# Kernel tuning notes

Hardware: AMD Instinct MI355X
Metric: run time of the kernel (lower is better)

## Reference

```python
import jax, jax.numpy as jnp
import numpy as np
from jax import lax

T = 256        # sentence length
V = 50000      # vocab
NT = 50        # POS tags
NL = 40        # dependency labels
WD, TD = 300, 100
IN = WD + TD   # 400, LSTM input & hidden size
H = IN
BI = 2 * H     # 800, biLSTM output per token
MI = 2 * BI    # 1600, MLP input/hidden size


def setup_inputs() -> dict:
    key = jax.random.key(0)
    ks = jax.random.split(key, 32)
    s = 0.05
    d = {
        'words': jax.random.randint(ks[0], (T,), 0, V),
        'tags': jax.random.randint(ks[1], (T,), 0, NT),
        'arcs': jax.random.randint(ks[2], (T + 1,), 0, T + 1),
        'h0': jax.random.normal(ks[3], (4, 1, H), jnp.float32),
        'c0': jax.random.normal(ks[4], (4, 1, H), jnp.float32),
        'word_emb': jax.random.normal(ks[5], (V, WD), jnp.float32) * s,
        'tag_emb': jax.random.normal(ks[6], (NT, TD), jnp.float32) * s,
        # LSTM layer 0: input IN; layer 1: input BI. Leading dim 2 = directions (fwd, rev).
        'Wih0': jax.random.normal(ks[7], (2, 4 * H, IN), jnp.float32) * s,
        'Whh0': jax.random.normal(ks[8], (2, 4 * H, H), jnp.float32) * s,
        'bih0': jax.random.normal(ks[9], (2, 4 * H), jnp.float32) * s,
        'bhh0': jax.random.normal(ks[10], (2, 4 * H), jnp.float32) * s,
        'Wih1': jax.random.normal(ks[11], (2, 4 * H, BI), jnp.float32) * s,
        'Whh1': jax.random.normal(ks[12], (2, 4 * H, H), jnp.float32) * s,
        'bih1': jax.random.normal(ks[13], (2, 4 * H), jnp.float32) * s,
        'bhh1': jax.random.normal(ks[14], (2, 4 * H), jnp.float32) * s,
        # arc-score MLP: 1600 -> 1600 -> 1 (Linear, Tanh, Linear)
        'Wa1': jax.random.normal(ks[15], (MI, MI), jnp.float32) * s,
        'ba1': jax.random.normal(ks[16], (MI,), jnp.float32) * s,
        'Wa2': jax.random.normal(ks[17], (1, MI), jnp.float32) * s,
        'ba2': jax.random.normal(ks[18], (1,), jnp.float32) * s,
        # label MLP: 1600 -> 1600 -> 40
        'Wl1': jax.random.normal(ks[19], (MI, MI), jnp.float32) * s,
        'bl1': jax.random.normal(ks[20], (MI,), jnp.float32) * s,
        'Wl2': jax.random.normal(ks[21], (NL, MI), jnp.float32) * s,
        'bl2': jax.random.normal(ks[22], (NL,), jnp.float32) * s,
    }
    return d


def _lstm_dir(x, Wih, Whh, bih, bhh, h, c):
    # x: [T, in]; returns [T, H]. Torch gate order i, f, g, o.
    xg = x @ Wih.T + (bih + bhh)  # precompute input projection: [T, 4H]

    def step(carry, xt):
        h, c = carry
        g = xt + h @ Whh.T
        i, f, gg, o = jnp.split(g, 4, axis=-1)
        i, f, o = jax.nn.sigmoid(i), jax.nn.sigmoid(f), jax.nn.sigmoid(o)
        c = f * c + i * jnp.tanh(gg)
        h = o * jnp.tanh(c)
        return (h, c), h

    (_, _), ys = lax.scan(step, (h, c), xg)
    return ys


def _bilstm_layer(x, Wih, Whh, bih, bhh, h0f, c0f, h0b, c0b):
    fwd = _lstm_dir(x, Wih[0], Whh[0], bih[0], bhh[0], h0f, c0f)
    bwd = _lstm_dir(x[::-1], Wih[1], Whh[1], bih[1], bhh[1], h0b, c0b)[::-1]
    return jnp.concatenate([fwd, bwd], axis=-1)


def _mlp(z, W1, b1, W2, b2):
    return jnp.tanh(z @ W1.T + b1) @ W2.T + b2


def reference(words, tags, arcs, h0, c0, word_emb, tag_emb,
              Wih0, Whh0, bih0, bhh0, Wih1, Whh1, bih1, bhh1,
              Wa1, ba1, Wa2, ba2, Wl1, bl1, Wl2, bl2):
    n = words.shape[0]
    x = jnp.concatenate([word_emb[words], tag_emb[tags]], axis=-1)  # [T, 400]
    x1 = _bilstm_layer(x, Wih0, Whh0, bih0, bhh0, h0[0, 0], c0[0, 0], h0[1, 0], c0[1, 0])
    hV = _bilstm_layer(x1, Wih1, Whh1, bih1, bhh1, h0[2, 0], c0[2, 0], h0[3, 0], c0[3, 0])  # [T, 800]

    # All-pairs arc scores: feats[h, d] = concat(hV[h], hV[d]) -> MLP -> scalar.
    hh = jnp.broadcast_to(hV[:, None, :], (n, n, BI))
    dd = jnp.broadcast_to(hV[None, :, :], (n, n, BI))
    feats = jnp.concatenate([hh, dd], axis=-1)  # [T, T, 1600]
    raw = _mlp(feats, Wa1, ba1, Wa2, ba2)[..., 0]  # [T, T]
    raw = raw * (1.0 - jnp.eye(n, dtype=raw.dtype))  # head == dep left at 0
    scores = jnp.zeros((n + 1, n + 1), raw.dtype).at[1:, 1:].set(raw).at[0, 0].set(1.0)

    # Labels: for token i with gold head h (1-based), concat(hV[i], hV[h-1]); head==0 -> zeros.
    heads = arcs[1:]
    idx = jnp.clip(heads - 1, 0, n - 1)
    lf = jnp.concatenate([hV, hV[idx]], axis=-1)  # [T, 1600]
    lab = _mlp(lf, Wl1, bl1, Wl2, bl2)  # [T, 40]
    lab = jnp.where((heads == 0)[:, None], jnp.zeros_like(lab), lab)
    return (scores, lab)
```

## Files before the change

kernel.cpp:

```cpp
#include <hip/hip_runtime.h>

typedef unsigned int   u32;
typedef unsigned long long u64;

__device__ __forceinline__ float fast_tanh(float x) {
    x = fminf(fmaxf(x, -15.f), 15.f);
    float e = __expf(2.f * x);
    return __fdividef(e - 1.f, e + 1.f);
}

#define HLD(p) __hip_atomic_load((p), __ATOMIC_RELAXED, __HIP_MEMORY_SCOPE_AGENT)

#define OF_XG   ((size_t)0)
#define OF_H    (OF_XG + 3276800)
#define OF_PQ   (OF_H  + 1638400)
#define OF_U    (OF_PQ + 3276800)

struct H4 { u64 v0, v1, v2, v3; const u64* p; u32 want; };

__device__ __forceinline__ H4 h4_issue(const u64* __restrict__ hist, int t, int k, u32 base) {
    H4 h;
    if (k < 400) { h.p = hist + (size_t)t * 400 + k;                          h.want = base + (u32)t + 1u; }
    else         { h.p = hist + 102400 + (size_t)(255 - t) * 400 + (k - 400); h.want = base + (u32)(255 - t) + 1u; }
    h.v0 = HLD(h.p + 0); h.v1 = HLD(h.p + 1); h.v2 = HLD(h.p + 2); h.v3 = HLD(h.p + 3);
    return h;
}

__device__ __forceinline__ float4 h4_fin(H4 h) {
    while ((u32)(h.v0 >> 32) != h.want || (u32)(h.v1 >> 32) != h.want ||
           (u32)(h.v2 >> 32) != h.want || (u32)(h.v3 >> 32) != h.want) {
        __builtin_amdgcn_s_sleep(4);
        h.v0 = HLD(h.p + 0); h.v1 = HLD(h.p + 1); h.v2 = HLD(h.p + 2); h.v3 = HLD(h.p + 3);
    }
    return make_float4(__uint_as_float((u32)h.v0), __uint_as_float((u32)h.v1),
                       __uint_as_float((u32)h.v2), __uint_as_float((u32)h.v3));
}

__device__ __forceinline__ void gate_wait(const u64* __restrict__ w0, const u64* __restrict__ w1,
                                          u32 want0, u32 want1) {
    if (threadIdx.x == 0) {
        for (;;) {
            u32 g0 = (u32)(HLD(w0) >> 32);
            u32 g1 = (u32)(HLD(w1) >> 32);
            if (g0 == want0 && g1 == want1) break;
            __builtin_amdgcn_s_sleep(16);
        }
    }
    __syncthreads();
}

__device__ __forceinline__ void gate_cnt(const u32* __restrict__ c, u32 target) {
    if (threadIdx.x == 0) {
        while (__hip_atomic_load(c, __ATOMIC_RELAXED, __HIP_MEMORY_SCOPE_AGENT) < target)
            __builtin_amdgcn_s_sleep(16);
        (void)__hip_atomic_load(c, __ATOMIC_ACQUIRE, __HIP_MEMORY_SCOPE_AGENT);
    }
    __syncthreads();
}

__device__ __forceinline__ void stage_nb(float (*As)[68], float (*Bs)[68],
                                         int lk, int lr, float4 av, float4 bv) {
    As[lk + 0][lr] = av.x; As[lk + 1][lr] = av.y; As[lk + 2][lr] = av.z; As[lk + 3][lr] = av.w;
    Bs[lk + 0][lr] = bv.x; Bs[lk + 1][lr] = bv.y; Bs[lk + 2][lr] = bv.z; Bs[lk + 3][lr] = bv.w;
}

__device__ __forceinline__ void fma16(float acc[4][4], const float (*As)[68], const float (*Bs)[68],
                                      int tx, int ty) {
    #pragma unroll
    for (int kk = 0; kk < 16; ++kk) {
        float4 a4 = *(const float4*)&As[kk][ty * 4];
        float4 b4 = *(const float4*)&Bs[kk][tx * 4];
        acc[0][0] += a4.x * b4.x; acc[0][1] += a4.x * b4.y; acc[0][2] += a4.x * b4.z; acc[0][3] += a4.x * b4.w;
        acc[1][0] += a4.y * b4.x; acc[1][1] += a4.y * b4.y; acc[1][2] += a4.y * b4.z; acc[1][3] += a4.y * b4.w;
        acc[2][0] += a4.z * b4.x; acc[2][1] += a4.z * b4.y; acc[2][2] += a4.z * b4.z; acc[2][3] += a4.z * b4.w;
        acc[3][0] += a4.w * b4.x; acc[3][1] += a4.w * b4.y; acc[3][2] += a4.w * b4.z; acc[3][3] += a4.w * b4.w;
    }
}

__device__ __forceinline__ void gemm_seg(float (*AsB)[16][68], float (*BsB)[16][68],
        float acc[4][4], const u64* __restrict__ hist, int t, int tind, u32 base,
        const float* __restrict__ brow, int kb, int klen,
        int lk, int lr, int tx, int ty, int& pb)
{
    int ka = kb + lk;
    H4 h = h4_issue(hist, ka < 800 ? t : tind, ka < 800 ? ka : ka - 800, base);
    float4 bv = *(const float4*)(brow + ka);
    for (int k0 = kb; k0 < kb + klen; k0 += 16) {
        float4 av = h4_fin(h);
        stage_nb(AsB[pb], BsB[pb], lk, lr, av, bv);
        int kn = k0 + 16;
        if (kn < kb + klen) {
            int k2 = kn + lk;
            h  = h4_issue(hist, k2 < 800 ? t : tind, k2 < 800 ? k2 : k2 - 800, base);
            bv = *(const float4*)(brow + k2);
        }
        __syncthreads();
        fma16(acc, AsB[pb], BsB[pb], tx, ty);
        pb ^= 1;
    }
}

__global__ __launch_bounds__(256)
void gemm_embed_kernel(const int* __restrict__ words, const int* __restrict__ tags,
                       const float* __restrict__ wemb, const float* __restrict__ temb,
                       const float* __restrict__ B,
                       const float* __restrict__ bias1, const float* __restrict__ bias2,
                       float* __restrict__ C, u32* __restrict__ cnt) {
    int t0 = blockIdx.x * 64;
    int n0 = blockIdx.y * 64;
    int tid = threadIdx.x;
    if (blockIdx.x == 0 && blockIdx.y == 0 && tid < 4) cnt[tid] = 0u;
    int tx = tid & 15, ty = tid >> 4;
    int lr = tid >> 2, lk = (tid & 3) * 4;
    __shared__ float As[2][16][68];
    __shared__ float Bs[2][16][68];
    float acc[4][4] = {};

    int t = t0 + lr;
    const float* arow0 = wemb + (size_t)words[t] * 300;
    const float* arow1 = temb + (size_t)tags[t] * 100 - 300;
    const float* brow  = B + (size_t)(n0 + lr) * 400;

    int p = 0;
    float4 av, bv;
    { int k = lk; av = (k < 300) ? *(const float4*)(arow0 + k) : *(const float4*)(arow1 + k);
      bv = *(const float4*)(brow + k); }
    for (int k0 = 0; k0 < 400; k0 += 16) {
        stage_nb(As[p], Bs[p], lk, lr, av, bv);
        int kn = k0 + 16;
        if (kn < 400) {
            int k = kn + lk;
            av = (k < 300) ? *(const float4*)(arow0 + k) : *(const float4*)(arow1 + k);
            bv = *(const float4*)(brow + k);
        }
        __syncthreads();
        fma16(acc, As[p], Bs[p], tx, ty);
        p ^= 1;
    }
    float bs[4];
    #pragma unroll
    for (int j = 0; j < 4; ++j) {
        int n = n0 + tx * 4 + j;
        bs[j] = bias1[n] + bias2[n];
    }
    #pragma unroll
    for (int i = 0; i < 4; ++i) {
        int tr = t0 + ty * 4 + i;
        float4 o;
        o.x = acc[i][0] + bs[0]; o.y = acc[i][1] + bs[1];
        o.z = acc[i][2] + bs[2]; o.w = acc[i][3] + bs[3];
        *(float4*)(C + (size_t)tr * 3200 + n0 + tx * 4) = o;
    }
}

#define LSTM_G 50
__device__ __forceinline__ void lstm_body(int bid,
                 const float* __restrict__ Whh,
                 const float* __restrict__ h0,
                 const float* __restrict__ c0,
                 int hc_base,
                 const float* __restrict__ xg,
                 u64* __restrict__ hist,
                 u32 tag_base,
                 float (*hbuf)[416],
                 const u32* __restrict__ cnt) {
    const int T = 256;
    int d  = bid / LSTM_G;
    int wg = bid % LSTM_G;
    int a8 = wg * 8;
    int tid = threadIdx.x;
    int w = tid >> 6, lane = tid & 63;
    int c = lane & 7, r = lane >> 3;
    int gate = r >> 1, jj = r & 1;
    int gr = gate * 400 + a8 + 2 * w + jj;

    float4 wv[13];
    const float* wrow = Whh + (size_t)d * 640000 + (size_t)gr * 400;
    #pragma unroll
    for (int i = 0; i < 13; ++i) {
        int k = 4 * (c + 8 * i);
        wv[i] = (k + 3 < 400) ? *(const float4*)(wrow + k) : make_float4(0.f, 0.f, 0.f, 0.f);
    }
    if (tid < 16) { hbuf[0][400 + tid] = 0.f; hbuf[1][400 + tid] = 0.f; }

    float c_state = 0.f;
    if (lane == 0 || lane == 8)
        c_state = c0[(hc_base + d) * 400 + a8 + 2 * w + jj];

    if (cnt) { gate_cnt(&cnt[0], 50); gate_cnt(&cnt[1], 50); gate_cnt(&cnt[2], 50); gate_cnt(&cnt[3], 50); }

    u64* hst = hist + (size_t)d * 102400;
    bool need2 = (tid + 256 < 400);

    for (int t = 0; t < T; ++t) {
        int xt = d ? (T - 1 - t) : t;
        float xgv = xg[(size_t)xt * 3200 + d * 1600 + gr];
        float* hb = hbuf[t & 1];

        if (t == 0) {
            hb[tid] = h0[(hc_base + d) * 400 + tid];
            if (need2) hb[tid + 256] = h0[(hc_base + d) * 400 + tid + 256];
        } else {
            const u64* src = hst + (size_t)(t - 1) * 400;
            u32 want = tag_base + (u32)t;
            bool d1 = false, d2 = !need2;
            while (!(d1 && d2)) {
                u64 v1 = 0, v2 = 0;
                if (!d1) v1 = HLD(&src[tid]);
                if (!d2) v2 = HLD(&src[tid + 256]);
                if (!d1 && (u32)(v1 >> 32) == want) { hb[tid] = __uint_as_float((u32)v1); d1 = true; }
                if (!d2 && (u32)(v2 >> 32) == want) { hb[tid + 256] = __uint_as_float((u32)v2); d2 = true; }
            }
        }
        __syncthreads();

        const float4* h4 = (const float4*)hb;
        float s = 0.f;
        #pragma unroll
        for (int i = 0; i < 13; ++i) {
            float4 hv = h4[c + 8 * i];
            s += wv[i].x * hv.x + wv[i].y * hv.y + wv[i].z * hv.z + wv[i].w * hv.w;
        }
        s += __shfl_down(s, 4);
        s += __shfl_down(s, 2);
        s += __shfl_down(s, 1);

        float v = 0.f;
        if (c == 0) {
            float tot = s + xgv;
            float arg = (gate == 2) ? 2.f * tot : -tot;
            arg = fminf(fmaxf(arg, -60.f), 60.f);
            float e = __expf(arg);
            v = (gate == 2) ? (e - 1.f) * __frcp_rn(e + 1.f)
                            : __frcp_rn(1.f + e);
        }
        float fv = __shfl(v, lane + 16);
        float gv = __shfl(v, lane + 32);
        float ov = __shfl(v, lane + 48);
        if (lane == 0 || lane == 8) {
            c_state = fv * c_state + v * gv;
            float ec = __expf(fminf(fmaxf(2.f * c_state, -60.f), 60.f));
            float th = (ec - 1.f) * __frcp_rn(ec + 1.f);
            float h = ov * th;
            u64 pk = (((u64)(tag_base + t + 1)) << 32) | (u64)__float_as_uint(h);
            __hip_atomic_store(&hst[(size_t)t * 400 + a8 + 2 * w + jj], pk,
                               __ATOMIC_RELAXED, __HIP_MEMORY_SCOPE_AGENT);
        }
    }
}

union SmemU {
    struct { float As[2][16][68]; float Bs[2][16][68]; } g;
    float hbuf[2][416];
};

__global__ __launch_bounds__(256)
void mega_kernel(const float* __restrict__ Whh0, const float* __restrict__ Whh1,
                 const float* __restrict__ h0, const float* __restrict__ c0,
                 const float* __restrict__ xg0, float* __restrict__ xg1,
                 u64* __restrict__ hist, const int* __restrict__ arcs,
                 const float* __restrict__ Wih1, const float* __restrict__ bih1,
                 const float* __restrict__ bhh1,
                 const float* __restrict__ Wa1, const float* __restrict__ ba1,
                 const float* __restrict__ Wl1, const float* __restrict__ bl1,
                 float* __restrict__ PQ, float* __restrict__ U, u32* __restrict__ cnt) {
    __shared__ SmemU sm;
    int bid = blockIdx.x;
    int tid = threadIdx.x;

    if (bid < 100) {
        lstm_body(bid, Whh0, h0, c0, 0, xg0, hist, 0u, sm.hbuf, nullptr);
        return;
    }
    if (bid < 300) {
        int g = bid - 100;
        int t0 = (g & 3) * 64;
        int n0 = (g >> 2) * 64;
        int tx = tid & 15, ty = tid >> 4;
        int lr = tid >> 2, lk = (tid & 3) * 4;
        float acc[4][4] = {};
        int t = t0 + lr;
        const float* brow = Wih1 + (size_t)(n0 + lr) * 800;

        int first = (t0 >= 128) ? 400 : 0;
        int pb = 0;
        for (int seg = 0; seg < 2; ++seg) {
            int kb = first ^ (seg ? 400 : 0);
            if (kb == 0) {
                const u64* gw = hist + (size_t)(t0 + 63) * 400;
                gate_wait(gw, gw + 399, (u32)(t0 + 64), (u32)(t0 + 64));
            } else {
                const u64* gw = hist + 102400 + (size_t)(255 - t0) * 400;
                gate_wait(gw, gw + 399, (u32)(256 - t0), (u32)(256 - t0));
            }
            gemm_seg(sm.g.As, sm.g.Bs, acc, hist, t, t, 0u, brow, kb, 400, lk, lr, tx, ty, pb);
        }
        float bs[4];
        #pragma unroll
        for (int j = 0; j < 4; ++j) {
            int n = n0 + tx * 4 + j;
            bs[j] = bih1[n] + bhh1[n];
        }
        #pragma unroll
        for (int i = 0; i < 4; ++i) {
            int tr = t0 + ty * 4 + i;
            float4 o;
            o.x = acc[i][0] + bs[0]; o.y = acc[i][1] + bs[1];
            o.z = acc[i][2] + bs[2]; o.w = acc[i][3] + bs[3];
            *(float4*)(xg1 + (size_t)tr * 3200 + n0 + tx * 4) = o;
        }
        __syncthreads();
        if (tid == 0)
            __hip_atomic_fetch_add(&cnt[t0 >> 6], 1u, __ATOMIC_RELEASE, __HIP_MEMORY_SCOPE_AGENT);
        return;
    }
    if (bid < 400) {
        lstm_body(bid - 300, Whh1, h0, c0, 2, xg1, hist, 256u, sm.hbuf, cnt);
        return;
    }

    gate_cnt(&cnt[0], 50); gate_cnt(&cnt[1], 50); gate_cnt(&cnt[2], 50); gate_cnt(&cnt[3], 50);

    int tx = tid & 15, ty = tid >> 4;
    int lr = tid >> 2, lk = (tid & 3) * 4;
    float acc[4][4] = {};
    int pb = 0;

    if (bid < 500) {
        int g = bid - 400;
        int t0 = (g & 3) * 64;
        int n0 = (g >> 2) * 64;
        int t = t0 + lr;
        int first = (t0 >= 128) ? 400 : 0;
        int h = arcs[1 + t];
        int tind = min(max(h - 1, 0), 255);
        const float* brow = Wl1 + (size_t)(n0 + lr) * 1600;
        for (int seg = 0; seg < 3; ++seg) {
            int kb   = (seg < 2) ? (first ^ (seg ? 400 : 0)) : 800;
            int klen = (seg < 2) ? 400 : 800;
            if (seg < 2) {
                if (kb == 0) {
                    const u64* gw = hist + (size_t)(t0 + 63) * 400;
                    gate_wait(gw, gw + 399, (u32)(t0 + 320), (u32)(t0 + 320));
                } else {
                    const u64* gw = hist + 102400 + (size_t)(255 - t0) * 400;
                    gate_wait(gw, gw + 399, (u32)(512 - t0), (u32)(512 - t0));
                }
            } else {
                const u64* gf = hist + (size_t)255 * 400;
                const u64* gb = hist + 102400 + (size_t)255 * 400;
                gate_wait(gf, gb, 512u, 512u);
            }
            gemm_seg(sm.g.As, sm.g.Bs, acc, hist, t, tind, 256u, brow, kb, klen, lk, lr, tx, ty, pb);
        }
        float bs[4];
        #pragma unroll
        for (int j = 0; j < 4; ++j) bs[j] = bl1[n0 + tx * 4 + j];
        #pragma unroll
        for (int i = 0; i < 4; ++i) {
            int tr = t0 + ty * 4 + i;
            float4 o;
            o.x = fast_tanh(acc[i][0] + bs[0]); o.y = fast_tanh(acc[i][1] + bs[1]);
            o.z = fast_tanh(acc[i][2] + bs[2]); o.w = fast_tanh(acc[i][3] + bs[3]);
            *(float4*)(U + (size_t)tr * 1600 + n0 + tx * 4) = o;
        }
    } else {
        int g = bid - 500;
        int t0 = (g & 3) * 64;
        int n0 = (g >> 2) * 64;
        int t = t0 + lr;
        int first = (t0 >= 128) ? 400 : 0;
        int nn = n0 + lr;
        const float* brow = (nn < 1600) ? Wa1 + (size_t)nn * 1600
                                        : Wa1 + (size_t)(nn - 1600) * 1600 + 800;
        for (int seg = 0; seg < 2; ++seg) {
            int kb = first ^ (seg ? 400 : 0);
            if (kb == 0) {
                const u64* gw = hist + (size_t)(t0 + 63) * 400;
                gate_wait(gw, gw + 399, (u32)(t0 + 320), (u32)(t0 + 320));
            } else {
                const u64* gw = hist + 102400 + (size_t)(255 - t0) * 400;
                gate_wait(gw, gw + 399, (u32)(512 - t0), (u32)(512 - t0));
            }
            gemm_seg(sm.g.As, sm.g.Bs, acc, hist, t, t, 256u, brow, kb, 400, lk, lr, tx, ty, pb);
        }
        float bs[4];
        #pragma unroll
        for (int j = 0; j < 4; ++j) {
            int n = n0 + tx * 4 + j;
            bs[j] = (n < 1600) ? ba1[n] : 0.f;
        }
        #pragma unroll
        for (int i = 0; i < 4; ++i) {
            int tr = t0 + ty * 4 + i;
            float4 o;
            o.x = acc[i][0] + bs[0]; o.y = acc[i][1] + bs[1];
            o.z = acc[i][2] + bs[2]; o.w = acc[i][3] + bs[3];
            *(float4*)(PQ + (size_t)tr * 3200 + n0 + tx * 4) = o;
        }
    }
}

__global__ __launch_bounds__(256)
void arc_kernel(const float* __restrict__ PQ,
                const float* __restrict__ Wa2, const float* __restrict__ ba2,
                float* __restrict__ out) {
    int i0 = blockIdx.x * 8, j0 = blockIdx.y * 8;
    int tid = threadIdx.x;
    __shared__ float Pt[8][66], Qt[8][66];
    __shared__ float W2f[1600];
    __shared__ float part[4][64];

    if (blockIdx.x == 0 && blockIdx.y == 0) {
        if (tid < 257) out[tid] = (tid == 0) ? 1.0f : 0.0f;
        out[(size_t)(tid + 1) * 257] = 0.0f;
        if (tid == 0) out[0] = 1.0f;
    }
    for (int m = tid; m < 1600; m += 256) W2f[m] = Wa2[m];

    int out_i = tid & 63, ii = out_i >> 3, jj = out_i & 7, mc = tid >> 6;
    int slr = tid >> 5, slc = (tid & 31) * 2;
    float acc = 0.f;
    for (int m0 = 0; m0 < 1600; m0 += 64) {
        float2 pv = *(const float2*)(PQ + (size_t)(i0 + slr) * 3200 + m0 + slc);
        float2 qv = *(const float2*)(PQ + (size_t)(j0 + slr) * 3200 + 1600 + m0 + slc);
        __syncthreads();
        Pt[slr][slc] = pv.x; Pt[slr][slc + 1] = pv.y;
        Qt[slr][slc] = qv.x; Qt[slr][slc + 1] = qv.y;
        __syncthreads();
        #pragma unroll
        for (int mm = 0; mm < 16; ++mm) {
            int m = mc * 16 + mm;
            float s = Pt[ii][m] + Qt[jj][m];
            acc += W2f[m0 + m] * fast_tanh(s);
        }
    }
    part[mc][out_i] = acc;
    __syncthreads();
    if (tid < 64) {
        float raw = part[0][tid] + part[1][tid] + part[2][tid] + part[3][tid] + ba2[0];
        int gi = i0 + (tid >> 3), gj = j0 + (tid & 7);
        if (gi == gj) raw = 0.f;
        out[(size_t)(gi + 1) * 257 + (gj + 1)] = raw;
    }
}

__global__ __launch_bounds__(256)
void label_out_kernel(const float* __restrict__ U, const float* __restrict__ Wl2,
                      const float* __restrict__ bl2, const int* __restrict__ arcs,
                      float* __restrict__ out) {
    int t = blockIdx.x;
    __shared__ float u_l[1600];
    __shared__ float part[4][64];
    for (int m = threadIdx.x; m < 1600; m += 256) u_l[m] = U[(size_t)t * 1600 + m];
    __syncthreads();
    int tid = threadIdx.x;
    int n = tid & 63, p = tid >> 6;
    float acc = 0.f;
    if (n < 40) {
        const float4* wr4 = (const float4*)(Wl2 + (size_t)n * 1600 + p * 400);
        const float*  ub  = u_l + p * 400;
        for (int m = 0; m < 100; ++m) {
            float4 w = wr4[m];
            acc += ub[4*m] * w.x + ub[4*m+1] * w.y + ub[4*m+2] * w.z + ub[4*m+3] * w.w;
        }
    }
    part[p][n] = acc;
    __syncthreads();
    if (tid < 40) {
        float v = part[0][tid] + part[1][tid] + part[2][tid] + part[3][tid] + bl2[tid];
        if (arcs[1 + t] == 0) v = 0.f;
        out[(size_t)t * 40 + tid] = v;
    }
}

extern "C" void kernel_launch(void* const* d_in, const int* in_sizes, int n_in,
                              void* d_out, int out_size, void* d_ws, size_t ws_size,
                              hipStream_t stream) {
    const int*   words = (const int*)d_in[0];
    const int*   tags  = (const int*)d_in[1];
    const int*   arcs  = (const int*)d_in[2];
    const float* h0    = (const float*)d_in[3];
    const float* c0    = (const float*)d_in[4];
    const float* wemb  = (const float*)d_in[5];
    const float* temb  = (const float*)d_in[6];
    const float* Wih0  = (const float*)d_in[7];
    const float* Whh0  = (const float*)d_in[8];
    const float* bih0  = (const float*)d_in[9];
    const float* bhh0  = (const float*)d_in[10];
    const float* Wih1  = (const float*)d_in[11];
    const float* Whh1  = (const float*)d_in[12];
    const float* bih1  = (const float*)d_in[13];
    const float* bhh1  = (const float*)d_in[14];
    const float* Wa1   = (const float*)d_in[15];
    const float* ba1   = (const float*)d_in[16];
    const float* Wa2   = (const float*)d_in[17];
    const float* ba2   = (const float*)d_in[18];
    const float* Wl1   = (const float*)d_in[19];
    const float* bl1   = (const float*)d_in[20];
    const float* Wl2   = (const float*)d_in[21];
    const float* bl2   = (const float*)d_in[22];
    float* out = (float*)d_out;

    char* ws = (char*)d_ws;
    float* xg0  = (float*)(ws + OF_XG);
    u64*   hist = (u64*)  (ws + OF_H);
    float* xg1  = (float*)(ws + OF_PQ);
    float* PQ   = (float*)(ws + OF_XG);
    float* U    = (float*)(ws + OF_U);
    u32*   cnt  = (u32*)out + 66040;

    gemm_embed_kernel<<<dim3(4, 50), 256, 0, stream>>>(words, tags, wemb, temb, Wih0, bih0, bhh0, xg0, cnt);
    mega_kernel<<<700, 256, 0, stream>>>(Whh0, Whh1, h0, c0, xg0, xg1, hist, arcs,
                                         Wih1, bih1, bhh1, Wa1, ba1, Wl1, bl1, PQ, U, cnt);
    arc_kernel<<<dim3(32, 32), 256, 0, stream>>>(PQ, Wa2, ba2, out);
    label_out_kernel<<<256, 256, 0, stream>>>(U, Wl2, bl2, arcs, out + 66049);
}
```

Before: 1.137 ms.

## Fuse layer-0 input GEMM into mega kernel and split label MLP into per-token halves

The embedding and layer-0 input-projection GEMM moves into the persistent mega kernel as 200 extra blocks, each bumping a per-time-tile counter. The layer-0 LSTM waits on those counters per 64-step tile, so the recurrence can begin before the whole GEMM finishes. The label MLP first layer is rewritten the same way as the arc MLP: separate left and right projections per token, gathered and passed through tanh in the label output kernel. This drops the gated 800-wide gather segment and lets the label GEMM blocks run with the same two-segment schedule. The cost is a memset launch, a larger grid that depends on co-residency for the spin-waits, and a doubled label projection output.

New measurement: 1.129 ms. About the same (-0.8%).

```diff
diff --git a/kernel.cpp b/kernel.cpp
--- a/kernel.cpp
+++ b/kernel.cpp
@@ -14,7 +14,6 @@
 #define OF_XG   ((size_t)0)
 #define OF_H    (OF_XG + 3276800)
 #define OF_PQ   (OF_H  + 1638400)
-#define OF_U    (OF_PQ + 3276800)
 
 struct H4 { u64 v0, v1, v2, v3; const u64* p; u32 want; };
 
@@ -100,59 +99,6 @@
     }
 }
 
-__global__ __launch_bounds__(256)
-void gemm_embed_kernel(const int* __restrict__ words, const int* __restrict__ tags,
-                       const float* __restrict__ wemb, const float* __restrict__ temb,
-                       const float* __restrict__ B,
-                       const float* __restrict__ bias1, const float* __restrict__ bias2,
-                       float* __restrict__ C, u32* __restrict__ cnt) {
-    int t0 = blockIdx.x * 64;
-    int n0 = blockIdx.y * 64;
-    int tid = threadIdx.x;
-    if (blockIdx.x == 0 && blockIdx.y == 0 && tid < 4) cnt[tid] = 0u;
-    int tx = tid & 15, ty = tid >> 4;
-    int lr = tid >> 2, lk = (tid & 3) * 4;
-    __shared__ float As[2][16][68];
-    __shared__ float Bs[2][16][68];
-    float acc[4][4] = {};
-
-    int t = t0 + lr;
-    const float* arow0 = wemb + (size_t)words[t] * 300;
-    const float* arow1 = temb + (size_t)tags[t] * 100 - 300;
-    const float* brow  = B + (size_t)(n0 + lr) * 400;
-
-    int p = 0;
-    float4 av, bv;
-    { int k = lk; av = (k < 300) ? *(const float4*)(arow0 + k) : *(const float4*)(arow1 + k);
-      bv = *(const float4*)(brow + k); }
-    for (int k0 = 0; k0 < 400; k0 += 16) {
-        stage_nb(As[p], Bs[p], lk, lr, av, bv);
-        int kn = k0 + 16;
-        if (kn < 400) {
-            int k = kn + lk;
-            av = (k < 300) ? *(const float4*)(arow0 + k) : *(const float4*)(arow1 + k);
-            bv = *(const float4*)(brow + k);
-        }
-        __syncthreads();
-        fma16(acc, As[p], Bs[p], tx, ty);
-        p ^= 1;
-    }
-    float bs[4];
-    #pragma unroll
-    for (int j = 0; j < 4; ++j) {
-        int n = n0 + tx * 4 + j;
-        bs[j] = bias1[n] + bias2[n];
-    }
-    #pragma unroll
-    for (int i = 0; i < 4; ++i) {
-        int tr = t0 + ty * 4 + i;
-        float4 o;
-        o.x = acc[i][0] + bs[0]; o.y = acc[i][1] + bs[1];
-        o.z = acc[i][2] + bs[2]; o.w = acc[i][3] + bs[3];
-        *(float4*)(C + (size_t)tr * 3200 + n0 + tx * 4) = o;
-    }
-}
-
 #define LSTM_G 50
 __device__ __forceinline__ void lstm_body(int bid,
                  const float* __restrict__ Whh,
@@ -163,7 +109,8 @@
                  u64* __restrict__ hist,
                  u32 tag_base,
                  float (*hbuf)[416],
-                 const u32* __restrict__ cnt) {
+                 const u32* __restrict__ cntPre,
+                 const u32* __restrict__ cntXg) {
     const int T = 256;
     int d  = bid / LSTM_G;
     int wg = bid % LSTM_G;
@@ -187,12 +134,17 @@
     if (lane == 0 || lane == 8)
         c_state = c0[(hc_base + d) * 400 + a8 + 2 * w + jj];
 
-    if (cnt) { gate_cnt(&cnt[0], 50); gate_cnt(&cnt[1], 50); gate_cnt(&cnt[2], 50); gate_cnt(&cnt[3], 50); }
+    if (cntPre) { gate_cnt(&cntPre[0], 50); gate_cnt(&cntPre[1], 50);
+                  gate_cnt(&cntPre[2], 50); gate_cnt(&cntPre[3], 50); }
 
     u64* hst = hist + (size_t)d * 102400;
     bool need2 = (tid + 256 < 400);
 
     for (int t = 0; t < T; ++t) {
+        if (cntXg && (t & 63) == 0) {
+            int tile = d ? 3 - (t >> 6) : (t >> 6);
+            gate_cnt(&cntXg[tile], 50);
+        }
         int xt = d ? (T - 1 - t) : t;
         float xgv = xg[(size_t)xt * 3200 + d * 1600 + gr];
         float* hb = hbuf[t & 1];
@@ -255,29 +207,80 @@
 };
 
 __global__ __launch_bounds__(256)
-void mega_kernel(const float* __restrict__ Whh0, const float* __restrict__ Whh1,
+void mega_kernel(const int* __restrict__ words, const int* __restrict__ tags,
+                 const float* __restrict__ wemb, const float* __restrict__ temb,
+                 const float* __restrict__ Wih0, const float* __restrict__ bih0,
+                 const float* __restrict__ bhh0,
+                 const float* __restrict__ Whh0, const float* __restrict__ Whh1,
                  const float* __restrict__ h0, const float* __restrict__ c0,
-                 const float* __restrict__ xg0, float* __restrict__ xg1,
+                 float* __restrict__ xg0, float* __restrict__ xg1,
                  u64* __restrict__ hist, const int* __restrict__ arcs,
                  const float* __restrict__ Wih1, const float* __restrict__ bih1,
                  const float* __restrict__ bhh1,
                  const float* __restrict__ Wa1, const float* __restrict__ ba1,
-                 const float* __restrict__ Wl1, const float* __restrict__ bl1,
-                 float* __restrict__ PQ, float* __restrict__ U, u32* __restrict__ cnt) {
+                 const float* __restrict__ Wl1,
+                 float* __restrict__ PQ, float* __restrict__ ULVR,
+                 u32* __restrict__ cnt) {
     __shared__ SmemU sm;
     int bid = blockIdx.x;
     int tid = threadIdx.x;
-
-    if (bid < 100) {
-        lstm_body(bid, Whh0, h0, c0, 0, xg0, hist, 0u, sm.hbuf, nullptr);
+    int tx = tid & 15, ty = tid >> 4;
+    int lr = tid >> 2, lk = (tid & 3) * 4;
+
+    if (bid < 200) {
+        int ttile, nt;
+        if (bid < 100) { ttile = (bid & 1) * 3;  nt = bid >> 1; }
+        else           { ttile = 1 + (bid & 1);  nt = (bid - 100) >> 1; }
+        int t0 = ttile * 64, n0 = nt * 64;
+        float acc[4][4] = {};
+        int t = t0 + lr;
+        const float* arow0 = wemb + (size_t)words[t] * 300;
+        const float* arow1 = temb + (size_t)tags[t] * 100 - 300;
+        const float* brow  = Wih0 + (size_t)(n0 + lr) * 400;
+
+        int p = 0;
+        float4 av, bv;
+        { int k = lk; av = (k < 300) ? *(const float4*)(arow0 + k) : *(const float4*)(arow1 + k);
+          bv = *(const float4*)(brow + k); }
+        for (int k0 = 0; k0 < 400; k0 += 16) {
+            stage_nb(sm.g.As[p], sm.g.Bs[p], lk, lr, av, bv);
+            int kn = k0 + 16;
+            if (kn < 400) {
+                int k = kn + lk;
+                av = (k < 300) ? *(const float4*)(arow0 + k) : *(const float4*)(arow1 + k);
+                bv = *(const float4*)(brow + k);
+            }
+            __syncthreads();
+            fma16(acc, sm.g.As[p], sm.g.Bs[p], tx, ty);
+            p ^= 1;
+        }
+        float bs[4];
+        #pragma unroll
+        for (int j = 0; j < 4; ++j) {
+            int n = n0 + tx * 4 + j;
+            bs[j] = bih0[n] + bhh0[n];
+        }
+        #pragma unroll
+        for (int i = 0; i < 4; ++i) {
+            int tr = t0 + ty * 4 + i;
+            float4 o;
+            o.x = acc[i][0] + bs[0]; o.y = acc[i][1] + bs[1];
+            o.z = acc[i][2] + bs[2]; o.w = acc[i][3] + bs[3];
+            *(float4*)(xg0 + (size_t)tr * 3200 + n0 + tx * 4) = o;
+        }
+        __syncthreads();
+        if (tid == 0)
+            __hip_atomic_fetch_add(&cnt[4 + ttile], 1u, __ATOMIC_RELEASE, __HIP_MEMORY_SCOPE_AGENT);
         return;
     }
     if (bid < 300) {
-        int g = bid - 100;
+        lstm_body(bid - 200, Whh0, h0, c0, 0, xg0, hist, 0u, sm.hbuf, nullptr, cnt + 4);
+        return;
+    }
+    if (bid < 500) {
+        int g = bid - 300;
         int t0 = (g & 3) * 64;
         int n0 = (g >> 2) * 64;
-        int tx = tid & 15, ty = tid >> 4;
-        int lr = tid >> 2, lk = (tid & 3) * 4;
         float acc[4][4] = {};
         int t = t0 + lr;
         const float* brow = Wih1 + (size_t)(n0 + lr) * 800;
@@ -314,90 +317,56 @@
             __hip_atomic_fetch_add(&cnt[t0 >> 6], 1u, __ATOMIC_RELEASE, __HIP_MEMORY_SCOPE_AGENT);
         return;
     }
-    if (bid < 400) {
-        lstm_body(bid - 300, Whh1, h0, c0, 2, xg1, hist, 256u, sm.hbuf, cnt);
+    if (bid < 600) {
+        lstm_body(bid - 500, Whh1, h0, c0, 2, xg1, hist, 256u, sm.hbuf, cnt, nullptr);
         return;
     }
 
     gate_cnt(&cnt[0], 50); gate_cnt(&cnt[1], 50); gate_cnt(&cnt[2], 50); gate_cnt(&cnt[3], 50);
 
-    int tx = tid & 15, ty = tid >> 4;
-    int lr = tid >> 2, lk = (tid & 3) * 4;
     float acc[4][4] = {};
     int pb = 0;
-
-    if (bid < 500) {
-        int g = bid - 400;
-        int t0 = (g & 3) * 64;
-        int n0 = (g >> 2) * 64;
-        int t = t0 + lr;
-        int first = (t0 >= 128) ? 400 : 0;
-        int h = arcs[1 + t];
-        int tind = min(max(h - 1, 0), 255);
-        const float* brow = Wl1 + (size_t)(n0 + lr) * 1600;
-        for (int seg = 0; seg < 3; ++seg) {
-            int kb   = (seg < 2) ? (first ^ (seg ? 400 : 0)) : 800;
-            int klen = (seg < 2) ? 400 : 800;
-            if (seg < 2) {
-                if (kb == 0) {
-                    const u64* gw = hist + (size_t)(t0 + 63) * 400;
-                    gate_wait(gw, gw + 399, (u32)(t0 + 320), (u32)(t0 + 320));
-                } else {
-                    const u64* gw = hist + 102400 + (size_t)(255 - t0) * 400;
-                    gate_wait(gw, gw + 399, (u32)(512 - t0), (u32)(512 - t0));
-                }
-            } else {
-                const u64* gf = hist + (size_t)255 * 400;
-                const u64* gb = hist + 102400 + (size_t)255 * 400;
-                gate_wait(gf, gb, 512u, 512u);
-            }
-            gemm_seg(sm.g.As, sm.g.Bs, acc, hist, t, tind, 256u, brow, kb, klen, lk, lr, tx, ty, pb);
-        }
-        float bs[4];
-        #pragma unroll
-        for (int j = 0; j < 4; ++j) bs[j] = bl1[n0 + tx * 4 + j];
-        #pragma unroll
-        for (int i = 0; i < 4; ++i) {
-            int tr = t0 + ty * 4 + i;
-            float4 o;
-            o.x = fast_tanh(acc[i][0] + bs[0]); o.y = fast_tanh(acc[i][1] + bs[1]);
-            o.z = fast_tanh(acc[i][2] + bs[2]); o.w = fast_tanh(acc[i][3] + bs[3]);
-            *(float4*)(U + (size_t)tr * 1600 + n0 + tx * 4) = o;
-        }
-    } else {
-        int g = bid - 500;
-        int t0 = (g & 3) * 64;
-        int n0 = (g >> 2) * 64;
-        int t = t0 + lr;
-        int first = (t0 >= 128) ? 400 : 0;
-        int nn = n0 + lr;
-        const float* brow = (nn < 1600) ? Wa1 + (size_t)nn * 1600
-                                        : Wa1 + (size_t)(nn - 1600) * 1600 + 800;
-        for (int seg = 0; seg < 2; ++seg) {
-            int kb = first ^ (seg ? 400 : 0);
-            if (kb == 0) {
-                const u64* gw = hist + (size_t)(t0 + 63) * 400;
-                gate_wait(gw, gw + 399, (u32)(t0 + 320), (u32)(t0 + 320));
-            } else {
-                const u64* gw = hist + 102400 + (size_t)(255 - t0) * 400;
-                gate_wait(gw, gw + 399, (u32)(512 - t0), (u32)(512 - t0));
-            }
-            gemm_seg(sm.g.As, sm.g.Bs, acc, hist, t, t, 256u, brow, kb, 400, lk, lr, tx, ty, pb);
-        }
-        float bs[4];
+    int g  = (bid < 800) ? bid - 600 : bid - 800;
+    int t0 = (g & 3) * 64;
+    int n0 = (g >> 2) * 64;
+    int t = t0 + lr;
+    int first = (t0 >= 128) ? 400 : 0;
+    int nn = n0 + lr;
+    const float* W  = (bid < 800) ? Wa1 : Wl1;
+    const float* brow = (nn < 1600) ? W + (size_t)nn * 1600
+                                    : W + (size_t)(nn - 1600) * 1600 + 800;
+    for (int seg = 0; seg < 2; ++seg) {
+        int kb = first ^ (seg ? 400 : 0);
+        if (kb == 0) {
+            const u64* gw = hist + (size_t)(t0 + 63) * 400;
+            gate_wait(gw, gw + 399, (u32)(t0 + 320), (u32)(t0 + 320));
+        } else {
+            const u64* gw = hist + 102400 + (size_t)(255 - t0) * 400;
+            gate_wait(gw, gw + 399, (u32)(512 - t0), (u32)(512 - t0));
+        }
+        gemm_seg(sm.g.As, sm.g.Bs, acc, hist, t, t, 256u, brow, kb, 400, lk, lr, tx, ty, pb);
+    }
+    float bs[4];
+    float* dst;
+    if (bid < 800) {
         #pragma unroll
         for (int j = 0; j < 4; ++j) {
             int n = n0 + tx * 4 + j;
             bs[j] = (n < 1600) ? ba1[n] : 0.f;
         }
-        #pragma unroll
-        for (int i = 0; i < 4; ++i) {
-            int tr = t0 + ty * 4 + i;
-            float4 o;
-            o.x = acc[i][0] + bs[0]; o.y = acc[i][1] + bs[1];
-            o.z = acc[i][2] + bs[2]; o.w = acc[i][3] + bs[3];
-            *(float4*)(PQ + (size_t)tr * 3200 + n0 + tx * 4) = o;
-        }
+        dst = PQ;
+    } else {
+        #pragma unroll
+        for (int j = 0; j < 4; ++j) bs[j] = 0.f;
+        dst = ULVR;
+    }
+    #pragma unroll
+    for (int i = 0; i < 4; ++i) {
+        int tr = t0 + ty * 4 + i;
+        float4 o;
+        o.x = acc[i][0] + bs[0]; o.y = acc[i][1] + bs[1];
+        o.z = acc[i][2] + bs[2]; o.w = acc[i][3] + bs[3];
+        *(float4*)(dst + (size_t)tr * 3200 + n0 + tx * 4) = o;
     }
 }
 
@@ -446,15 +415,20 @@
 }
 
 __global__ __launch_bounds__(256)
-void label_out_kernel(const float* __restrict__ U, const float* __restrict__ Wl2,
-                      const float* __restrict__ bl2, const int* __restrict__ arcs,
-                      float* __restrict__ out) {
+void label_out_kernel(const float* __restrict__ ULVR, const float* __restrict__ Wl2,
+                      const float* __restrict__ bl2, const float* __restrict__ bl1,
+                      const int* __restrict__ arcs, float* __restrict__ out) {
     int t = blockIdx.x;
     __shared__ float u_l[1600];
     __shared__ float part[4][64];
-    for (int m = threadIdx.x; m < 1600; m += 256) u_l[m] = U[(size_t)t * 1600 + m];
+    int tid = threadIdx.x;
+    int h = arcs[1 + t];
+    int tind = min(max(h - 1, 0), 255);
+    const float* ua = ULVR + (size_t)t * 3200;
+    const float* ur = ULVR + (size_t)tind * 3200 + 1600;
+    for (int m = tid; m < 1600; m += 256)
+        u_l[m] = fast_tanh(ua[m] + ur[m] + bl1[m]);
     __syncthreads();
-    int tid = threadIdx.x;
     int n = tid & 63, p = tid >> 6;
     float acc = 0.f;
     if (n < 40) {
@@ -507,12 +481,13 @@
     u64*   hist = (u64*)  (ws + OF_H);
     float* xg1  = (float*)(ws + OF_PQ);
     float* PQ   = (float*)(ws + OF_XG);
-    float* U    = (float*)(ws + OF_U);
+    float* ULVR = (float*)(ws + OF_PQ);
     u32*   cnt  = (u32*)out + 66040;
 
-    gemm_embed_kernel<<<dim3(4, 50), 256, 0, stream>>>(words, tags, wemb, temb, Wih0, bih0, bhh0, xg0, cnt);
-    mega_kernel<<<700, 256, 0, stream>>>(Whh0, Whh1, h0, c0, xg0, xg1, hist, arcs,
-                                         Wih1, bih1, bhh1, Wa1, ba1, Wl1, bl1, PQ, U, cnt);
+    hipMemsetAsync(cnt, 0, 32, stream);
+    mega_kernel<<<1000, 256, 0, stream>>>(words, tags, wemb, temb, Wih0, bih0, bhh0,
+                                          Whh0, Whh1, h0, c0, xg0, xg1, hist, arcs,
+                                          Wih1, bih1, bhh1, Wa1, ba1, Wl1, PQ, ULVR, cnt);
     arc_kernel<<<dim3(32, 32), 256, 0, stream>>>(PQ, Wa2, ba2, out);
-    label_out_kernel<<<256, 256, 0, stream>>>(U, Wl2, bl2, arcs, out + 66049);
-}
+    label_out_kernel<<<256, 256, 0, stream>>>(ULVR, Wl2, bl2, bl1, arcs, out + 66049);
+}
```
